# Kernel tuning notes

Measured on AMD Instinct MI355X. Metric: run time of the kernel, lower is better.

Reference implementation:

```python
import jax, jax.numpy as jnp
import numpy as np
import math

N_HEAD = 8
LN_EPS = 1e-5


def _layernorm(x, g, b):
    mu = jnp.mean(x, axis=-1, keepdims=True)
    var = jnp.mean(jnp.square(x - mu), axis=-1, keepdims=True)
    return (x - mu) / jnp.sqrt(var + LN_EPS) * g + b


def setup_inputs() -> dict:
    key0 = jax.random.key(0)
    ks = jax.random.split(key0, 12)
    B, L, D, E = 4, 512, 256, 5  # batch, agents, n_embd, edge_feats_dim

    def w(k, shape):
        return jax.random.normal(k, shape, dtype=jnp.float32) * 0.02

    return {
        "key": jax.random.normal(ks[0], (B, L, D), jnp.float32),
        "value": jax.random.normal(ks[1], (B, L, D), jnp.float32),
        "query": jax.random.normal(ks[2], (B, L, D), jnp.float32),
        "atten_masks": jax.random.randint(ks[3], (B, L, L), 0, 2).astype(jnp.int32),
        "edge_feats": jax.random.normal(ks[4], (B, L, L, E), jnp.float32),
        # Linear weights stored [in, out] so forward is x @ W + b
        "Wk": w(ks[5], (D, D)), "bk": jnp.zeros((D,), jnp.float32),
        "Wq": w(ks[6], (D, D)), "bq": jnp.zeros((D,), jnp.float32),
        "Wv": w(ks[7], (D, D)), "bv": jnp.zeros((D,), jnp.float32),
        "Wp": w(ks[8], (D, D)), "bp": jnp.zeros((D,), jnp.float32),
        "We1": w(ks[9], (E, D)), "be1": jnp.zeros((D,), jnp.float32),
        "ln_g": jnp.ones((D,), jnp.float32), "ln_b": jnp.zeros((D,), jnp.float32),
        "We2": w(ks[10], (D, N_HEAD)), "be2": jnp.zeros((N_HEAD,), jnp.float32),
    }


def reference(key, value, query, atten_masks, edge_feats,
              Wk, bk, Wq, bq, Wv, bv, Wp, bp,
              We1, be1, ln_g, ln_b, We2, be2):
    B, L, D = query.shape
    hd = D // N_HEAD
    # QKV projections -> [B, H, L, hd]
    q = (query @ Wq + bq).reshape(B, L, N_HEAD, hd).transpose(0, 2, 1, 3)
    k = (key @ Wk + bk).reshape(B, L, N_HEAD, hd).transpose(0, 2, 1, 3)
    v = (value @ Wv + bv).reshape(B, L, N_HEAD, hd).transpose(0, 2, 1, 3)
    # scaled attention scores [B, H, L, L]
    att = jnp.einsum('bhqd,bhkd->bhqk', q, k) * (1.0 / math.sqrt(hd))
    # edge-feature additive bias: Linear -> ReLU -> LayerNorm -> Linear(per-head)
    e = jax.nn.relu(edge_feats @ We1 + be1)          # [B, L, L, D]
    e = _layernorm(e, ln_g, ln_b)
    e = e @ We2 + be2                                # [B, L, L, H]
    att = att + e.transpose(0, 3, 1, 2)
    # additive mask (0 -> -inf), softmax over keys
    att = jnp.where(atten_masks[:, None, :, :] == 0, -jnp.inf, att)
    att = jax.nn.softmax(att, axis=-1)
    y = jnp.einsum('bhqk,bhkd->bhqd', att, v)        # [B, H, L, hd]
    y = y.transpose(0, 2, 1, 3).reshape(B, L, D)
    return y @ Wp + bp
```

## Files before the change

### kernel.cpp

```cpp
#include <hip/hip_runtime.h>
#include <hip/hip_bf16.h>

#define L_SEQ 512
#define D_EMB 256
#define NH 8
#define HD 32
#define LL (L_SEQ * L_SEQ)

typedef __attribute__((ext_vector_type(8))) short short8;
typedef __attribute__((ext_vector_type(4))) float f32x4;
typedef unsigned short ushort;

__device__ __forceinline__ float bf2f(ushort u) {
    unsigned int x = ((unsigned int)u) << 16;
    float f;
    __builtin_memcpy(&f, &x, 4);
    return f;
}
__device__ __forceinline__ ushort f2bf(float x) {
    __hip_bfloat16 h = __float2bfloat16(x);
    ushort u;
    __builtin_memcpy(&u, &h, 2);
    return u;
}
__device__ __forceinline__ unsigned int fbits(float x) {
    unsigned int u;
    __builtin_memcpy(&u, &x, 4);
    return u;
}
__device__ __forceinline__ float asf(unsigned int u) {
    float f;
    __builtin_memcpy(&f, &u, 4);
    return f;
}
__device__ __forceinline__ unsigned int cvt_pk_bf16(float a, float b) {
    unsigned int r;
    asm("v_cvt_pk_bf16_f32 %0, %1, %2" : "=v"(r) : "v"(a), "v"(b));
    return r;
}
__device__ __forceinline__ unsigned int packhi(unsigned int y, unsigned int x) {
    return __builtin_amdgcn_perm(y, x, 0x07060302u);
}
__device__ __forceinline__ uint2 cvt_hilo2(float v0, float v1) {
    unsigned int hi = cvt_pk_bf16(v0, v1);
    float h0 = asf(hi << 16);
    float h1 = asf(hi & 0xffff0000u);
    unsigned int lo = cvt_pk_bf16(v0 - h0, v1 - h1);
    uint2 r; r.x = hi; r.y = lo;
    return r;
}

__global__ __launch_bounds__(256) void prep_kernel(
    const float* __restrict__ We1, const float* __restrict__ be1,
    const float* __restrict__ g,   const float* __restrict__ bta,
    const float* __restrict__ We2, const float* __restrict__ be2,
    const float* __restrict__ Wq, const float* __restrict__ Wk,
    const float* __restrict__ Wv, const float* __restrict__ Wp,
    ushort* __restrict__ W1G, ushort* __restrict__ B2G, float* __restrict__ tail,
    ushort* __restrict__ WThi, ushort* __restrict__ WTlo)
{
    int t = threadIdx.x;
    if (blockIdx.x != 0) {
        int bx = blockIdx.x - 1;
        int w = bx >> 4, ny = bx & 15;
        const float* W = (w == 0) ? Wq : (w == 1) ? Wk : (w == 2) ? Wv : Wp;
        ushort* dh = WThi + (size_t)w * 65536;
        ushort* dl = WTlo + (size_t)w * 65536;
        int n = ny * 16 + (t >> 4);
        int k0 = (t & 15) * 16;
        ushort hbuf[16], lbuf[16];
#pragma unroll
        for (int kk = 0; kk < 16; ++kk) {
            float v = W[(size_t)(k0 + kk) * 256 + n];
            unsigned int hb = fbits(v) + 0x8000u;
            ushort hi = (ushort)(hb >> 16);
            float res = v - bf2f(hi);
            hbuf[kk] = hi;
            lbuf[kk] = (ushort)((fbits(res) + 0x8000u) >> 16);
        }
        *(short8*)(dh + (size_t)n * 256 + k0)     = *(short8*)&hbuf[0];
        *(short8*)(dh + (size_t)n * 256 + k0 + 8) = *(short8*)&hbuf[8];
        *(short8*)(dl + (size_t)n * 256 + k0)     = *(short8*)&lbuf[0];
        *(short8*)(dl + (size_t)n * 256 + k0 + 8) = *(short8*)&lbuf[8];
        return;
    }

    __shared__ float red[16][256];
    float gd = g[t], bd = bta[t];
#pragma unroll
    for (int h = 0; h < 8; ++h) {
        float w2 = We2[t * 8 + h];
        red[h][t] = gd * w2;
        red[8 + h][t] = bd * w2;
    }
    __syncthreads();
    for (int off = 128; off > 0; off >>= 1) {
        if (t < off) {
#pragma unroll
            for (int row = 0; row < 16; ++row) red[row][t] += red[row][t + off];
        }
        __syncthreads();
    }
    if (t < 8) {
        tail[t] = red[t][0];
        tail[8 + t] = red[8 + t][0] + be2[t];
    }
    if (t >= 16 && t < 32) tail[t] = 0.f;

    for (int idx = t; idx < 8192; idx += 256) {
        int j = idx & 7, lane = (idx >> 3) & 63, tile = idx >> 9;
        int m = lane & 15, q = lane >> 4;
        int k = q * 8 + j;
        int d = (m >> 2) * 64 + tile * 4 + (m & 3);
        float v = 0.f;
        bool lo = false;
        if (k < 5)        v = We1[k * 256 + d];
        else if (k < 10)  { v = We1[(k - 5) * 256 + d]; lo = true; }
        else if (k < 15)  v = We1[(k - 10) * 256 + d];
        else if (k == 15) v = be1[d];
        else if (k == 16) { v = be1[d]; lo = true; }
        ushort hi = f2bf(v);
        W1G[idx] = lo ? f2bf(v - bf2f(hi)) : hi;
    }
    for (int idx = t; idx < 4096; idx += 256) {
        int j = idx & 7, lane = (idx >> 3) & 63, kc = idx >> 9;
        int n = lane & 15, q = lane >> 4;
        int d = q * 64 + kc * 8 + j;
        ushort out;
        if (n < 8)       out = f2bf(g[d] * We2[d * 8 + n]);
        else if (n == 8) out = 0x3F80;
        else             out = 0;
        B2G[idx] = out;
    }
}

__device__ __forceinline__ void gemm_body(
    const float* __restrict__ A, const ushort* __restrict__ BH,
    const ushort* __restrict__ BL, const float* __restrict__ bias,
    float* __restrict__ C, float* __restrict__ Ct,
    int bx, int by, char* smem)
{
    ushort* Ahi = (ushort*)smem;
    ushort* Alo = (ushort*)(smem + 5120);

    int tid = threadIdx.x;
    int wv = tid >> 6, lane = tid & 63;
    int m = lane & 15, quad = lane >> 4;
    int bm = bx * 64, bn = by * 64;

    int sm = tid >> 2, sg = (tid & 3) * 8;
    const float* Arow = A + (size_t)(bm + sm) * 256 + sg;

    int nrow = bn + wv * 16 + m;
    const ushort* bhp = BH + (size_t)nrow * 256 + quad * 8;
    const ushort* blp = BL + (size_t)nrow * 256 + quad * 8;

    f32x4 acc[4];
#pragma unroll
    for (int mt = 0; mt < 4; ++mt) acc[mt] = (f32x4){0.f, 0.f, 0.f, 0.f};

    for (int k0 = 0; k0 < 256; k0 += 32) {
        float4 a0 = *(const float4*)(Arow + k0);
        float4 a1 = *(const float4*)(Arow + k0 + 4);
        uint2 c0 = cvt_hilo2(a0.x, a0.y);
        uint2 c1 = cvt_hilo2(a0.z, a0.w);
        uint2 c2 = cvt_hilo2(a1.x, a1.y);
        uint2 c3 = cvt_hilo2(a1.z, a1.w);
        if (k0) __syncthreads();
        uint4 hq; hq.x = c0.x; hq.y = c1.x; hq.z = c2.x; hq.w = c3.x;
        uint4 lq; lq.x = c0.y; lq.y = c1.y; lq.z = c2.y; lq.w = c3.y;
        *(uint4*)&Ahi[sm * 40 + sg] = hq;
        *(uint4*)&Alo[sm * 40 + sg] = lq;
        __syncthreads();

        short8 bhi = *(const short8*)(bhp + k0);
        short8 blo = *(const short8*)(blp + k0);
#pragma unroll
        for (int mt = 0; mt < 4; ++mt) {
            short8 ahi = *(const short8*)&Ahi[(mt * 16 + m) * 40 + quad * 8];
            short8 alo = *(const short8*)&Alo[(mt * 16 + m) * 40 + quad * 8];
            acc[mt] = __builtin_amdgcn_mfma_f32_16x16x32_bf16(ahi, blo, acc[mt], 0, 0, 0);
            acc[mt] = __builtin_amdgcn_mfma_f32_16x16x32_bf16(alo, bhi, acc[mt], 0, 0, 0);
            acc[mt] = __builtin_amdgcn_mfma_f32_16x16x32_bf16(ahi, bhi, acc[mt], 0, 0, 0);
        }
    }

    float bn_bias = bias[nrow];
    if (Ct) {
        int bb = bm >> 9, l0 = bm & 511;
        float* outp = Ct + ((size_t)(bb * 256 + nrow)) * 512 + l0 + quad * 4;
#pragma unroll
        for (int mt = 0; mt < 4; ++mt) {
            float4 o;
            o.x = acc[mt][0] + bn_bias; o.y = acc[mt][1] + bn_bias;
            o.z = acc[mt][2] + bn_bias; o.w = acc[mt][3] + bn_bias;
            *(float4*)(outp + mt * 16) = o;
        }
    } else {
#pragma unroll
        for (int mt = 0; mt < 4; ++mt) {
#pragma unroll
            for (int r = 0; r < 4; ++r) {
                C[(size_t)(bm + mt * 16 + quad * 4 + r) * 256 + nrow] = acc[mt][r] + bn_bias;
            }
        }
    }
}

__device__ __forceinline__ void edge_body(
    const float* __restrict__ EF, const ushort* __restrict__ W1G,
    const ushort* __restrict__ B2G, const float* __restrict__ tail,
    ushort* __restrict__ E2, int bi)
{
    int tid = threadIdx.x;
    int wv = tid >> 6, lane = tid & 63;
    int q = lane >> 4, n = lane & 15;

    int b = bi >> 9, i = bi & 511;
    size_t rowbase = (size_t)bi * 512;

    short8 w1f[16];
#pragma unroll
    for (int t = 0; t < 16; ++t)
        w1f[t] = *(const short8*)(W1G + (t * 64 + lane) * 8);
    short8 b2f[8];
#pragma unroll
    for (int kc = 0; kc < 8; ++kc)
        b2f[kc] = *(const short8*)(B2G + (kc * 64 + lane) * 8);

    float shv = tail[n];
    float bbv = tail[8 + n];
    const float inv256 = 1.0f / 256.0f;

    const float* efbase = EF + rowbase * 5;
    int pairoff = wv * 16 + n;

    float4 evA = *(const float4*)(efbase + (size_t)pairoff * 5);
    float  evB = efbase[(size_t)pairoff * 5 + 4];

    for (int iter = 0; iter < 8; ++iter) {
        float4 nA; float nB;
        if (iter < 7) {
            const float* p = efbase + (size_t)((iter + 1) * 64 + pairoff) * 5;
            nA = *(const float4*)p;
            nB = p[4];
        }
        int jb = iter * 64 + wv * 16;

        unsigned int hb[5], la[5];
        hb[0] = fbits(evA.x); hb[1] = fbits(evA.y); hb[2] = fbits(evA.z);
        hb[3] = fbits(evA.w); hb[4] = fbits(evB);
        {
            float e0 = evA.x - asf(hb[0] & 0xffff0000u);
            float e1 = evA.y - asf(hb[1] & 0xffff0000u);
            float e2 = evA.z - asf(hb[2] & 0xffff0000u);
            float e3 = evA.w - asf(hb[3] & 0xffff0000u);
            float e4 = evB   - asf(hb[4] & 0xffff0000u);
            la[0] = fbits(e0) + 0x8000u;
            la[1] = fbits(e1) + 0x8000u;
            la[2] = fbits(e2) + 0x8000u;
            la[3] = fbits(e3) + 0x8000u;
            la[4] = fbits(e4) + 0x8000u;
        }
        unsigned int A0v = packhi(hb[1], hb[0]);
        unsigned int A1v = packhi(hb[3], hb[2]);
        unsigned int A2v = packhi(hb[0], hb[4]);
        unsigned int A3v = packhi(hb[2], hb[1]);
        unsigned int B0v = packhi(hb[4], hb[3]);
        unsigned int B1v = packhi(la[1], la[0]);
        unsigned int B2v = packhi(la[3], la[2]);
        unsigned int B3v = packhi(0x3F800000u, la[4]);
        uint4 efd;
        bool isq0 = (q == 0), isq1 = (q == 1), isq2 = (q == 2);
        efd.x = isq0 ? A0v : isq1 ? B0v : isq2 ? 0x3F80u : 0u;
        efd.y = isq0 ? A1v : isq1 ? B1v : 0u;
        efd.z = isq0 ? A2v : isq1 ? B2v : 0u;
        efd.w = isq0 ? A3v : isq1 ? B3v : 0u;
        short8 ef8;
        __builtin_memcpy(&ef8, &efd, 16);

        const f32x4 z = {0.f, 0.f, 0.f, 0.f};
        f32x4 acc  = z, acc2  = z;
        f32x4 accB = z, acc2B = z;
#pragma unroll
        for (int kc = 0; kc < 8; ++kc) {
            f32x4 dA = __builtin_amdgcn_mfma_f32_16x16x32_bf16(w1f[2 * kc],     ef8, z, 0, 0, 0);
            f32x4 dB = __builtin_amdgcn_mfma_f32_16x16x32_bf16(w1f[2 * kc + 1], ef8, z, 0, 0, 0);
            uint4 av;
            av.x = cvt_pk_bf16(fmaxf(dA[0], 0.f), fmaxf(dA[1], 0.f));
            av.y = cvt_pk_bf16(fmaxf(dA[2], 0.f), fmaxf(dA[3], 0.f));
            av.z = cvt_pk_bf16(fmaxf(dB[0], 0.f), fmaxf(dB[1], 0.f));
            av.w = cvt_pk_bf16(fmaxf(dB[2], 0.f), fmaxf(dB[3], 0.f));
            short8 a;
            __builtin_memcpy(&a, &av, 16);
            if (kc & 1) {
                accB  = __builtin_amdgcn_mfma_f32_16x16x32_bf16(a, b2f[kc], accB, 0, 0, 0);
                acc2B = __builtin_amdgcn_mfma_f32_16x16x32_bf16(a, a,       acc2B, 0, 0, 0);
            } else {
                acc  = __builtin_amdgcn_mfma_f32_16x16x32_bf16(a, b2f[kc], acc, 0, 0, 0);
                acc2 = __builtin_amdgcn_mfma_f32_16x16x32_bf16(a, a,       acc2, 0, 0, 0);
            }
        }
        acc  = acc + accB;
        acc2 = acc2 + acc2B;

        int base = lane & 48;
        float er[4];
#pragma unroll
        for (int r = 0; r < 4; ++r) {
            float sm = __shfl(acc[r], base + 8);
            float sq = __shfl(acc2[r], base + (base >> 2) + r);
            float dot = acc[r];
            float mu = sm * inv256;
            float var = fmaf(-mu, mu, sq * inv256);
            float rs = rsqrtf(var + 1e-5f);
            er[r] = fmaf(dot - mu * shv, rs, bbv);
        }
        if (n < 8) {
            uint2 outv;
            outv.x = cvt_pk_bf16(er[0], er[1]);
            outv.y = cvt_pk_bf16(er[2], er[3]);
            size_t basep = (((size_t)(b * NH + n) * L_SEQ + i) * L_SEQ) + jb + q * 4;
            *(uint2*)(E2 + basep) = outv;
        }
        evA = nA; evB = nB;
    }
}

__global__ __launch_bounds__(256) void fused_qkv_edge(
    const float* __restrict__ query, const float* __restrict__ key,
    const float* __restrict__ value,
    const ushort* __restrict__ WThi, const ushort* __restrict__ WTlo,
    const float* __restrict__ bq, const float* __restrict__ bk,
    const float* __restrict__ bv,
    float* __restrict__ Qw, float* __restrict__ Ktw, float* __restrict__ Vw,
    const float* __restrict__ EF, const ushort* __restrict__ W1G,
    const ushort* __restrict__ B2G, const float* __restrict__ tail,
    ushort* __restrict__ E2)
{
    __shared__ __align__(16) char smem[10240];
    int bid = blockIdx.x;
    if (bid < 384) {
        int z = bid >> 7, rem = bid & 127;
        int bx = rem & 31, by = rem >> 5;
        if (z == 0)
            gemm_body(query, WThi + 0 * 65536, WTlo + 0 * 65536, bq, Qw, nullptr, bx, by, smem);
        else if (z == 1)
            gemm_body(key,   WThi + 1 * 65536, WTlo + 1 * 65536, bk, nullptr, Ktw, bx, by, smem);
        else
            gemm_body(value, WThi + 2 * 65536, WTlo + 2 * 65536, bv, Vw, nullptr, bx, by, smem);
    } else {
        edge_body(EF, W1G, B2G, tail, E2, bid - 384);
    }
}

__global__ __launch_bounds__(256) void gemm_out(
    const float* __restrict__ A, const ushort* __restrict__ BH,
    const ushort* __restrict__ BL, const float* __restrict__ bias,
    float* __restrict__ C)
{
    __shared__ __align__(16) char smem[10240];
    gemm_body(A, BH, BL, bias, C, nullptr, blockIdx.x, blockIdx.y, smem);
}

__global__ __launch_bounds__(256, 4) void attn_kernel(
    const float* __restrict__ Q, const float* __restrict__ Kt,
    const float* __restrict__ V, const ushort* __restrict__ E2,
    const int* __restrict__ MSK, float* __restrict__ Y)
{
    __shared__ float stage[4096];
    __shared__ ushort pbuf[4][512][4];

    int bh = blockIdx.x;
    int b = bh >> 3, h = bh & 7;
    int tid = threadIdx.x;
    int wv = tid >> 6, lane = tid & 63;
    int i0 = blockIdx.y * 16;
    int i = i0 + wv * 4;

    const float* Ktb = Kt + (size_t)bh * (HD * L_SEQ);
    const float* Vb  = V + (size_t)b * L_SEQ * D_EMB + h * HD;

    int wvu = __builtin_amdgcn_readfirstlane(wv);
    const float* Qs = Q + ((size_t)(b * L_SEQ + i0 + wvu * 4)) * 256 + h * HD;

    size_t erow = ((size_t)bh * L_SEQ + i) * L_SEQ;
    size_t mrow = ((size_t)b * L_SEQ + i) * L_SEQ;

    unsigned int e2p[4][4];
    int2 mkp[4][4];
#pragma unroll
    for (int r = 0; r < 4; ++r)
#pragma unroll
        for (int c = 0; c < 4; ++c) {
            int j = c * 128 + 2 * lane;
            e2p[r][c] = *(const unsigned int*)(E2 + erow + (size_t)r * L_SEQ + j);
            mkp[r][c] = *(const int2*)(MSK + mrow + (size_t)r * L_SEQ + j);
        }

    float s[4][8];
#pragma unroll
    for (int r = 0; r < 4; ++r)
#pragma unroll
        for (int t = 0; t < 8; ++t) s[r][t] = 0.f;

    for (int c = 0; c < 4; ++c) {
        if (c) __syncthreads();
        {
            int d0 = tid >> 5, jj = (tid & 31) * 4;
#pragma unroll
            for (int p = 0; p < 4; ++p) {
                int d = p * 8 + d0;
                float4 kv = *(const float4*)(Ktb + (size_t)d * L_SEQ + c * 128 + jj);
                *(float4*)&stage[d * 128 + jj] = kv;
            }
        }
        __syncthreads();
        int c2 = c * 2;
#pragma unroll
        for (int d = 0; d < HD; ++d) {
            float q0 = Qs[0 * 256 + d];
            float q1 = Qs[1 * 256 + d];
            float q2 = Qs[2 * 256 + d];
            float q3 = Qs[3 * 256 + d];
            float2 kv = *(const float2*)&stage[d * 128 + 2 * lane];
            s[0][c2]     = fmaf(q0, kv.x, s[0][c2]);
            s[0][c2 + 1] = fmaf(q0, kv.y, s[0][c2 + 1]);
            s[1][c2]     = fmaf(q1, kv.x, s[1][c2]);
            s[1][c2 + 1] = fmaf(q1, kv.y, s[1][c2 + 1]);
            s[2][c2]     = fmaf(q2, kv.x, s[2][c2]);
            s[2][c2 + 1] = fmaf(q2, kv.y, s[2][c2 + 1]);
            s[3][c2]     = fmaf(q3, kv.x, s[3][c2]);
            s[3][c2 + 1] = fmaf(q3, kv.y, s[3][c2 + 1]);
        }
    }

    const float scl = 0.17677669529663687f;
#pragma unroll
    for (int r = 0; r < 4; ++r) {
        float m = -3.0e38f;
#pragma unroll
        for (int idx = 0; idx < 8; ++idx) {
            int c = idx >> 1, u = idx & 1;
            unsigned int pk = e2p[r][c];
            float e = bf2f((ushort)(u ? (pk >> 16) : (pk & 0xffff)));
            int mk = u ? mkp[r][c].y : mkp[r][c].x;
            float v = (mk != 0) ? fmaf(s[r][idx], scl, e) : -1e30f;
            s[r][idx] = v;
            m = fmaxf(m, v);
        }
#pragma unroll
        for (int o = 32; o > 0; o >>= 1) m = fmaxf(m, __shfl_xor(m, o));
        float ssum = 0.f;
#pragma unroll
        for (int idx = 0; idx < 8; ++idx) {
            float p = __expf(s[r][idx] - m);
            s[r][idx] = p;
            ssum += p;
        }
#pragma unroll
        for (int o = 32; o > 0; o >>= 1) ssum += __shfl_xor(ssum, o);
        float inv = 1.0f / ssum;
#pragma unroll
        for (int idx = 0; idx < 8; ++idx) s[r][idx] *= inv;
    }
#pragma unroll
    for (int c = 0; c < 4; ++c) {
        int c2 = c * 2;
        uint4 w;
        w.x = cvt_pk_bf16(s[0][c2],     s[1][c2]);
        w.y = cvt_pk_bf16(s[2][c2],     s[3][c2]);
        w.z = cvt_pk_bf16(s[0][c2 + 1], s[1][c2 + 1]);
        w.w = cvt_pk_bf16(s[2][c2 + 1], s[3][c2 + 1]);
        *(uint4*)&pbuf[wv][c * 128 + 2 * lane][0] = w;
    }

    int dg = lane >> 3, js = lane & 7;
    float4 acc[4];
#pragma unroll
    for (int r = 0; r < 4; ++r) { acc[r].x = 0.f; acc[r].y = 0.f; acc[r].z = 0.f; acc[r].w = 0.f; }

    for (int c = 0; c < 4; ++c) {
        __syncthreads();
        {
            int j0 = tid >> 3, dd = (tid & 7) * 4;
#pragma unroll
            for (int p = 0; p < 4; ++p) {
                int j = p * 32 + j0;
                float4 vv = *(const float4*)(Vb + (size_t)(c * 128 + j) * D_EMB + dd);
                *(float4*)&stage[j * 32 + dd] = vv;
            }
        }
        __syncthreads();
#pragma unroll
        for (int jb = 0; jb < 16; ++jb) {
            int jj = jb * 8 + js;
            float4 v4 = *(const float4*)&stage[jj * 32 + dg * 4];
            uint2 pu = *(const uint2*)&pbuf[wv][c * 128 + jj][0];
            float p0 = asf(pu.x << 16);
            float p1 = asf(pu.x & 0xffff0000u);
            float p2 = asf(pu.y << 16);
            float p3 = asf(pu.y & 0xffff0000u);
            acc[0].x = fmaf(p0, v4.x, acc[0].x);
            acc[0].y = fmaf(p0, v4.y, acc[0].y);
            acc[0].z = fmaf(p0, v4.z, acc[0].z);
            acc[0].w = fmaf(p0, v4.w, acc[0].w);
            acc[1].x = fmaf(p1, v4.x, acc[1].x);
            acc[1].y = fmaf(p1, v4.y, acc[1].y);
            acc[1].z = fmaf(p1, v4.z, acc[1].z);
            acc[1].w = fmaf(p1, v4.w, acc[1].w);
            acc[2].x = fmaf(p2, v4.x, acc[2].x);
            acc[2].y = fmaf(p2, v4.y, acc[2].y);
            acc[2].z = fmaf(p2, v4.z, acc[2].z);
            acc[2].w = fmaf(p2, v4.w, acc[2].w);
            acc[3].x = fmaf(p3, v4.x, acc[3].x);
            acc[3].y = fmaf(p3, v4.y, acc[3].y);
            acc[3].z = fmaf(p3, v4.z, acc[3].z);
            acc[3].w = fmaf(p3, v4.w, acc[3].w);
        }
    }

#pragma unroll
    for (int off = 1; off < 8; off <<= 1) {
#pragma unroll
        for (int r = 0; r < 4; ++r) {
            acc[r].x += __shfl_xor(acc[r].x, off);
            acc[r].y += __shfl_xor(acc[r].y, off);
            acc[r].z += __shfl_xor(acc[r].z, off);
            acc[r].w += __shfl_xor(acc[r].w, off);
        }
    }
    if (js == 0) {
#pragma unroll
        for (int r = 0; r < 4; ++r)
            *(float4*)(Y + ((size_t)(b * L_SEQ + i + r)) * 256 + h * HD + dg * 4) = acc[r];
    }
}

extern "C" void kernel_launch(void* const* d_in, const int* in_sizes, int n_in,
                              void* d_out, int out_size, void* d_ws, size_t ws_size,
                              hipStream_t stream)
{
    const float* key   = (const float*)d_in[0];
    const float* value = (const float*)d_in[1];
    const float* query = (const float*)d_in[2];
    const int*   msk   = (const int*)d_in[3];
    const float* ef    = (const float*)d_in[4];
    const float* Wk  = (const float*)d_in[5];  const float* bk  = (const float*)d_in[6];
    const float* Wq  = (const float*)d_in[7];  const float* bq  = (const float*)d_in[8];
    const float* Wv  = (const float*)d_in[9];  const float* bv  = (const float*)d_in[10];
    const float* Wp  = (const float*)d_in[11]; const float* bp  = (const float*)d_in[12];
    const float* We1 = (const float*)d_in[13]; const float* be1 = (const float*)d_in[14];
    const float* lng = (const float*)d_in[15]; const float* lnb = (const float*)d_in[16];
    const float* We2 = (const float*)d_in[17]; const float* be2 = (const float*)d_in[18];

    const int MTOK = 4 * L_SEQ;
    const int NELT = MTOK * D_EMB;

    float* ws    = (float*)d_ws;
    float* Qw    = ws;
    float* Vw    = Qw + NELT;
    float* Yw    = Vw + NELT;
    float* Ktw   = Yw + NELT;
    ushort* W1G  = (ushort*)(Ktw + NELT);
    ushort* B2G  = W1G + 8192;
    float* tail  = (float*)(B2G + 4096);
    ushort* WThi = (ushort*)(tail + 32);
    ushort* WTlo = WThi + 4 * 65536;
    ushort* E2   = WTlo + 4 * 65536;

    hipLaunchKernelGGL(prep_kernel, dim3(65), dim3(256), 0, stream,
                       We1, be1, lng, lnb, We2, be2,
                       Wq, Wk, Wv, Wp,
                       W1G, B2G, tail, WThi, WTlo);
    hipLaunchKernelGGL(fused_qkv_edge, dim3(2432), dim3(256), 0, stream,
                       query, key, value, WThi, WTlo, bq, bk, bv,
                       Qw, Ktw, Vw,
                       ef, W1G, B2G, tail, E2);
    hipLaunchKernelGGL(attn_kernel, dim3(32, 32), dim3(256), 0, stream,
                       Qw, Ktw, Vw, E2, msk, Yw);
    hipLaunchKernelGGL(gemm_out, dim3(32, 4), dim3(256), 0, stream,
                       Yw, WThi + 3 * 65536, WTlo + 3 * 65536, bp, (float*)d_out);
}
```

Before: 212.5 us.

## Stage edge MLP weights in LDS and process two pair tiles per iteration

The edge-bias path now copies the W1 and W2 MFMA fragments into shared memory once per block and reads them from LDS inside the loop, instead of holding 24 short8 fragments in registers. Each iteration handles two 16-pair tiles, interleaving their MFMA chains and halving the loop count. Launch bounds request 4 blocks per SM. The goal is to cut register pressure, raise occupancy and give the scheduler more independent MFMA work to hide latency. The cost is extra LDS traffic and a larger shared allocation (24 KB) that also applies to the GEMM blocks.

```diff
diff --git a/kernel.cpp b/kernel.cpp
--- a/kernel.cpp
+++ b/kernel.cpp
@@ -207,127 +207,152 @@
     }
 }
 
+__device__ __forceinline__ short8 make_ef8(const float4& evA, float evB, int q) {
+    unsigned int hb0 = fbits(evA.x), hb1 = fbits(evA.y), hb2 = fbits(evA.z),
+                 hb3 = fbits(evA.w), hb4 = fbits(evB);
+    float e0 = evA.x - asf(hb0 & 0xffff0000u);
+    float e1 = evA.y - asf(hb1 & 0xffff0000u);
+    float e2 = evA.z - asf(hb2 & 0xffff0000u);
+    float e3 = evA.w - asf(hb3 & 0xffff0000u);
+    float e4 = evB   - asf(hb4 & 0xffff0000u);
+    unsigned int la0 = fbits(e0) + 0x8000u;
+    unsigned int la1 = fbits(e1) + 0x8000u;
+    unsigned int la2 = fbits(e2) + 0x8000u;
+    unsigned int la3 = fbits(e3) + 0x8000u;
+    unsigned int la4 = fbits(e4) + 0x8000u;
+    unsigned int A0v = packhi(hb1, hb0);
+    unsigned int A1v = packhi(hb3, hb2);
+    unsigned int A2v = packhi(hb0, hb4);
+    unsigned int A3v = packhi(hb2, hb1);
+    unsigned int B0v = packhi(hb4, hb3);
+    unsigned int B1v = packhi(la1, la0);
+    unsigned int B2v = packhi(la3, la2);
+    unsigned int B3v = packhi(0x3F800000u, la4);
+    uint4 efd;
+    bool isq0 = (q == 0), isq1 = (q == 1), isq2 = (q == 2);
+    efd.x = isq0 ? A0v : isq1 ? B0v : isq2 ? 0x3F80u : 0u;
+    efd.y = isq0 ? A1v : isq1 ? B1v : 0u;
+    efd.z = isq0 ? A2v : isq1 ? B2v : 0u;
+    efd.w = isq0 ? A3v : isq1 ? B3v : 0u;
+    short8 ef8;
+    __builtin_memcpy(&ef8, &efd, 16);
+    return ef8;
+}
+
+__device__ __forceinline__ void ln_store(
+    const f32x4& acc, const f32x4& acc2, float shv, float bbv,
+    int lane, int n, int q, ushort* __restrict__ E2,
+    int b, int i, int jb)
+{
+    const float inv256 = 1.0f / 256.0f;
+    int base = lane & 48;
+    float er[4];
+#pragma unroll
+    for (int r = 0; r < 4; ++r) {
+        float sm = __shfl(acc[r], base + 8);
+        float sq = __shfl(acc2[r], base + (base >> 2) + r);
+        float dot = acc[r];
+        float mu = sm * inv256;
+        float var = fmaf(-mu, mu, sq * inv256);
+        float rs = rsqrtf(var + 1e-5f);
+        er[r] = fmaf(dot - mu * shv, rs, bbv);
+    }
+    if (n < 8) {
+        uint2 outv;
+        outv.x = cvt_pk_bf16(er[0], er[1]);
+        outv.y = cvt_pk_bf16(er[2], er[3]);
+        size_t basep = (((size_t)(b * NH + n) * L_SEQ + i) * L_SEQ) + jb + q * 4;
+        *(uint2*)(E2 + basep) = outv;
+    }
+}
+
 __device__ __forceinline__ void edge_body(
     const float* __restrict__ EF, const ushort* __restrict__ W1G,
     const ushort* __restrict__ B2G, const float* __restrict__ tail,
-    ushort* __restrict__ E2, int bi)
+    ushort* __restrict__ E2, int bi, char* smem)
 {
     int tid = threadIdx.x;
+    {
+        const uint4* s1 = (const uint4*)W1G;
+        uint4* d1 = (uint4*)smem;
+#pragma unroll
+        for (int k = 0; k < 4; ++k) d1[tid + k * 256] = s1[tid + k * 256];
+        const uint4* s2 = (const uint4*)B2G;
+        uint4* d2 = (uint4*)(smem + 16384);
+#pragma unroll
+        for (int k = 0; k < 2; ++k) d2[tid + k * 256] = s2[tid + k * 256];
+    }
     int wv = tid >> 6, lane = tid & 63;
     int q = lane >> 4, n = lane & 15;
 
     int b = bi >> 9, i = bi & 511;
     size_t rowbase = (size_t)bi * 512;
 
-    short8 w1f[16];
-#pragma unroll
-    for (int t = 0; t < 16; ++t)
-        w1f[t] = *(const short8*)(W1G + (t * 64 + lane) * 8);
-    short8 b2f[8];
-#pragma unroll
-    for (int kc = 0; kc < 8; ++kc)
-        b2f[kc] = *(const short8*)(B2G + (kc * 64 + lane) * 8);
-
     float shv = tail[n];
     float bbv = tail[8 + n];
-    const float inv256 = 1.0f / 256.0f;
 
     const float* efbase = EF + rowbase * 5;
-    int pairoff = wv * 16 + n;
-
-    float4 evA = *(const float4*)(efbase + (size_t)pairoff * 5);
-    float  evB = efbase[(size_t)pairoff * 5 + 4];
-
-    for (int iter = 0; iter < 8; ++iter) {
-        float4 nA; float nB;
-        if (iter < 7) {
-            const float* p = efbase + (size_t)((iter + 1) * 64 + pairoff) * 5;
-            nA = *(const float4*)p;
-            nB = p[4];
-        }
-        int jb = iter * 64 + wv * 16;
-
-        unsigned int hb[5], la[5];
-        hb[0] = fbits(evA.x); hb[1] = fbits(evA.y); hb[2] = fbits(evA.z);
-        hb[3] = fbits(evA.w); hb[4] = fbits(evB);
-        {
-            float e0 = evA.x - asf(hb[0] & 0xffff0000u);
-            float e1 = evA.y - asf(hb[1] & 0xffff0000u);
-            float e2 = evA.z - asf(hb[2] & 0xffff0000u);
-            float e3 = evA.w - asf(hb[3] & 0xffff0000u);
-            float e4 = evB   - asf(hb[4] & 0xffff0000u);
-            la[0] = fbits(e0) + 0x8000u;
-            la[1] = fbits(e1) + 0x8000u;
-            la[2] = fbits(e2) + 0x8000u;
-            la[3] = fbits(e3) + 0x8000u;
-            la[4] = fbits(e4) + 0x8000u;
-        }
-        unsigned int A0v = packhi(hb[1], hb[0]);
-        unsigned int A1v = packhi(hb[3], hb[2]);
-        unsigned int A2v = packhi(hb[0], hb[4]);
-        unsigned int A3v = packhi(hb[2], hb[1]);
-        unsigned int B0v = packhi(hb[4], hb[3]);
-        unsigned int B1v = packhi(la[1], la[0]);
-        unsigned int B2v = packhi(la[3], la[2]);
-        unsigned int B3v = packhi(0x3F800000u, la[4]);
-        uint4 efd;
-        bool isq0 = (q == 0), isq1 = (q == 1), isq2 = (q == 2);
-        efd.x = isq0 ? A0v : isq1 ? B0v : isq2 ? 0x3F80u : 0u;
-        efd.y = isq0 ? A1v : isq1 ? B1v : 0u;
-        efd.z = isq0 ? A2v : isq1 ? B2v : 0u;
-        efd.w = isq0 ? A3v : isq1 ? B3v : 0u;
-        short8 ef8;
-        __builtin_memcpy(&ef8, &efd, 16);
-
-        const f32x4 z = {0.f, 0.f, 0.f, 0.f};
-        f32x4 acc  = z, acc2  = z;
-        f32x4 accB = z, acc2B = z;
+    int pair0 = wv * 32 + n;
+
+    const float* p0 = efbase + (size_t)pair0 * 5;
+    float4 evA0 = *(const float4*)p0;        float evB0 = p0[4];
+    float4 evA1 = *(const float4*)(p0 + 80); float evB1 = p0[84];
+
+    __syncthreads();
+    const short8* w1l = (const short8*)smem;
+    const short8* b2l = (const short8*)(smem + 16384);
+
+    const f32x4 z = {0.f, 0.f, 0.f, 0.f};
+
+    for (int iter = 0; iter < 4; ++iter) {
+        float4 nA0, nA1; float nB0 = 0.f, nB1 = 0.f;
+        if (iter < 3) {
+            const float* pn = efbase + (size_t)((iter + 1) * 128 + pair0) * 5;
+            nA0 = *(const float4*)pn;        nB0 = pn[4];
+            nA1 = *(const float4*)(pn + 80); nB1 = pn[84];
+        }
+        int jb0 = iter * 128 + wv * 32;
+
+        short8 ef0 = make_ef8(evA0, evB0, q);
+        short8 ef1 = make_ef8(evA1, evB1, q);
+
+        f32x4 acc0 = z, acc20 = z, acc1 = z, acc21 = z;
 #pragma unroll
         for (int kc = 0; kc < 8; ++kc) {
-            f32x4 dA = __builtin_amdgcn_mfma_f32_16x16x32_bf16(w1f[2 * kc],     ef8, z, 0, 0, 0);
-            f32x4 dB = __builtin_amdgcn_mfma_f32_16x16x32_bf16(w1f[2 * kc + 1], ef8, z, 0, 0, 0);
-            uint4 av;
-            av.x = cvt_pk_bf16(fmaxf(dA[0], 0.f), fmaxf(dA[1], 0.f));
-            av.y = cvt_pk_bf16(fmaxf(dA[2], 0.f), fmaxf(dA[3], 0.f));
-            av.z = cvt_pk_bf16(fmaxf(dB[0], 0.f), fmaxf(dB[1], 0.f));
-            av.w = cvt_pk_bf16(fmaxf(dB[2], 0.f), fmaxf(dB[3], 0.f));
-            short8 a;
-            __builtin_memcpy(&a, &av, 16);
-            if (kc & 1) {
-                accB  = __builtin_amdgcn_mfma_f32_16x16x32_bf16(a, b2f[kc], accB, 0, 0, 0);
-                acc2B = __builtin_amdgcn_mfma_f32_16x16x32_bf16(a, a,       acc2B, 0, 0, 0);
-            } else {
-                acc  = __builtin_amdgcn_mfma_f32_16x16x32_bf16(a, b2f[kc], acc, 0, 0, 0);
-                acc2 = __builtin_amdgcn_mfma_f32_16x16x32_bf16(a, a,       acc2, 0, 0, 0);
-            }
-        }
-        acc  = acc + accB;
-        acc2 = acc2 + acc2B;
-
-        int base = lane & 48;
-        float er[4];
-#pragma unroll
-        for (int r = 0; r < 4; ++r) {
-            float sm = __shfl(acc[r], base + 8);
-            float sq = __shfl(acc2[r], base + (base >> 2) + r);
-            float dot = acc[r];
-            float mu = sm * inv256;
-            float var = fmaf(-mu, mu, sq * inv256);
-            float rs = rsqrtf(var + 1e-5f);
-            er[r] = fmaf(dot - mu * shv, rs, bbv);
-        }
-        if (n < 8) {
-            uint2 outv;
-            outv.x = cvt_pk_bf16(er[0], er[1]);
-            outv.y = cvt_pk_bf16(er[2], er[3]);
-            size_t basep = (((size_t)(b * NH + n) * L_SEQ + i) * L_SEQ) + jb + q * 4;
-            *(uint2*)(E2 + basep) = outv;
-        }
-        evA = nA; evB = nB;
-    }
-}
-
-__global__ __launch_bounds__(256) void fused_qkv_edge(
+            short8 wa = w1l[2 * kc * 64 + lane];
+            short8 wb = w1l[(2 * kc + 1) * 64 + lane];
+            short8 b2 = b2l[kc * 64 + lane];
+            f32x4 dA0 = __builtin_amdgcn_mfma_f32_16x16x32_bf16(wa, ef0, z, 0, 0, 0);
+            f32x4 dB0 = __builtin_amdgcn_mfma_f32_16x16x32_bf16(wb, ef0, z, 0, 0, 0);
+            f32x4 dA1 = __builtin_amdgcn_mfma_f32_16x16x32_bf16(wa, ef1, z, 0, 0, 0);
+            f32x4 dB1 = __builtin_amdgcn_mfma_f32_16x16x32_bf16(wb, ef1, z, 0, 0, 0);
+            uint4 av0, av1;
+            av0.x = cvt_pk_bf16(fmaxf(dA0[0], 0.f), fmaxf(dA0[1], 0.f));
+            av0.y = cvt_pk_bf16(fmaxf(dA0[2], 0.f), fmaxf(dA0[3], 0.f));
+            av0.z = cvt_pk_bf16(fmaxf(dB0[0], 0.f), fmaxf(dB0[1], 0.f));
+            av0.w = cvt_pk_bf16(fmaxf(dB0[2], 0.f), fmaxf(dB0[3], 0.f));
+            av1.x = cvt_pk_bf16(fmaxf(dA1[0], 0.f), fmaxf(dA1[1], 0.f));
+            av1.y = cvt_pk_bf16(fmaxf(dA1[2], 0.f), fmaxf(dA1[3], 0.f));
+            av1.z = cvt_pk_bf16(fmaxf(dB1[0], 0.f), fmaxf(dB1[1], 0.f));
+            av1.w = cvt_pk_bf16(fmaxf(dB1[2], 0.f), fmaxf(dB1[3], 0.f));
+            short8 a0, a1;
+            __builtin_memcpy(&a0, &av0, 16);
+            __builtin_memcpy(&a1, &av1, 16);
+            acc0  = __builtin_amdgcn_mfma_f32_16x16x32_bf16(a0, b2, acc0, 0, 0, 0);
+            acc20 = __builtin_amdgcn_mfma_f32_16x16x32_bf16(a0, a0, acc20, 0, 0, 0);
+            acc1  = __builtin_amdgcn_mfma_f32_16x16x32_bf16(a1, b2, acc1, 0, 0, 0);
+            acc21 = __builtin_amdgcn_mfma_f32_16x16x32_bf16(a1, a1, acc21, 0, 0, 0);
+        }
+
+        ln_store(acc0, acc20, shv, bbv, lane, n, q, E2, b, i, jb0);
+        ln_store(acc1, acc21, shv, bbv, lane, n, q, E2, b, i, jb0 + 16);
+
+        evA0 = nA0; evB0 = nB0;
+        evA1 = nA1; evB1 = nB1;
+    }
+}
+
+__global__ __launch_bounds__(256, 4) void fused_qkv_edge(
     const float* __restrict__ query, const float* __restrict__ key,
     const float* __restrict__ value,
     const ushort* __restrict__ WThi, const ushort* __restrict__ WTlo,
@@ -338,7 +363,7 @@
     const ushort* __restrict__ B2G, const float* __restrict__ tail,
     ushort* __restrict__ E2)
 {
-    __shared__ __align__(16) char smem[10240];
+    __shared__ __align__(16) char smem[24576];
     int bid = blockIdx.x;
     if (bid < 384) {
         int z = bid >> 7, rem = bid & 127;
@@ -350,7 +375,7 @@
         else
             gemm_body(value, WThi + 2 * 65536, WTlo + 2 * 65536, bv, Vw, nullptr, bx, by, smem);
     } else {
-        edge_body(EF, W1G, B2G, tail, E2, bid - 384);
+        edge_body(EF, W1G, B2G, tail, E2, bid - 384, smem);
     }
 }
 
```

Result: faster. 200.8 us (-5.5%).
